# Kernel optimization log

Hardware: AMD Instinct MI355X
Metric: run time of the kernel (lower is better)

Reference implementation:

```python
import jax, jax.numpy as jnp
import numpy as np

IN_FEATURES = 4096
OUT_FEATURES = 4096
NNZ = 1677721  # int(4096*4096*(1-0.9))


def setup_inputs() -> dict:
    key = jax.random.key(0)
    k1, k2, k3, k4 = jax.random.split(key, 4)
    x = jax.random.normal(k1, (4, 2048, IN_FEATURES), dtype=jnp.float32)
    bound = 1.0 / np.sqrt(IN_FEATURES)
    sparse_values = jax.random.uniform(k2, (NNZ,), minval=-bound, maxval=bound, dtype=jnp.float32)
    bias = jax.random.uniform(k3, (OUT_FEATURES,), minval=-bound, maxval=bound, dtype=jnp.float32)
    flat_idx = jnp.sort(jax.random.randint(k4, (NNZ,), 0, IN_FEATURES * OUT_FEATURES, dtype=jnp.int64))
    return {"x": x, "sparse_values": sparse_values, "bias": bias, "flat_idx": flat_idx}


def reference(x, sparse_values, bias, flat_idx):
    # Fixed COO pattern: row = flat // in_features, col = flat % in_features
    rows = flat_idx // IN_FEATURES
    cols = flat_idx % IN_FEATURES
    # Scatter-add == COO coalesce (duplicates summed). W: [out, in]
    W = jnp.zeros((OUT_FEATURES, IN_FEATURES), dtype=sparse_values.dtype).at[rows, cols].add(sparse_values)
    # y = x W^T + b  (matches torch.sparse.mm(W, x^T)^T + b)
    y = jnp.einsum('bsi,oi->bso', x, W) + bias
    return y.astype(x.dtype)
```

## Files before the change

### kernel.cpp

```cpp
#include <hip/hip_runtime.h>
#include <hip/hip_bf16.h>
#include <stdint.h>

#define IN_F 4096
#define OUT_F 4096

typedef __attribute__((ext_vector_type(8))) __bf16 bf16x8;
typedef __attribute__((ext_vector_type(4))) float f32x4;

__device__ __forceinline__ void gl_lds_16(const void* g, void* l) {
    __builtin_amdgcn_global_load_lds((const __attribute__((address_space(1))) void*)g,
                                     (__attribute__((address_space(3))) void*)l,
                                     16, 0, 0);
}

__global__ void cvt_and_scatter(const float* __restrict__ x, __bf16* __restrict__ Xb, int n8,
                                const float* __restrict__ vals, const int* __restrict__ idx,
                                __bf16* __restrict__ W, int nnz, int cvtBlocks) {
    if ((int)blockIdx.x < cvtBlocks) {
        int i = blockIdx.x * blockDim.x + threadIdx.x;
        if (i < n8) {
            const float4* src = (const float4*)(x + (size_t)i * 8);
            float4 v0 = src[0], v1 = src[1];
            bf16x8 o;
            o[0] = (__bf16)v0.x; o[1] = (__bf16)v0.y; o[2] = (__bf16)v0.z; o[3] = (__bf16)v0.w;
            o[4] = (__bf16)v1.x; o[5] = (__bf16)v1.y; o[6] = (__bf16)v1.z; o[7] = (__bf16)v1.w;
            *(bf16x8*)(Xb + (size_t)i * 8) = o;
        }
    } else {
        int i = (blockIdx.x - cvtBlocks) * blockDim.x + threadIdx.x;
        if (i >= nnz) return;
        const int id = idx[i];
        if (i > 0 && idx[i - 1] == id) return;
        float s = vals[i];
        for (int j = i + 1; j < nnz && idx[j] == id; ++j) s += vals[j];
        W[id] = (__bf16)s;
    }
}

#define BM 256
#define BN 256
#define BK 32
#define NT (IN_F / BK)

__global__ __launch_bounds__(512, 2) void gemm_bf16_bt(
    const __bf16* __restrict__ A, const __bf16* __restrict__ B,
    const float* __restrict__ bias, float* __restrict__ C,
    int M, int N, int K)
{
    __shared__ __align__(128) __bf16 lds[4][16384];

    const int t512 = threadIdx.x;
    const int wave = t512 >> 6;
    const int lane = t512 & 63;
    const int wm = wave >> 2;
    const int wn = wave & 3;
    const int lq = lane >> 4;
    const int lr = lane & 15;

    const int bid  = blockIdx.x;
    const int wgid = (bid & 7) * 64 + (bid >> 3);
    const int mt = wgid >> 4;
    const int nt = wgid & 15;
    const int tileM = mt * BM;
    const int tileN = nt * BN;

    const int srow = t512 >> 2;
    const int scol = ((t512 & 3) ^ ((t512 >> 3) & 3)) * 8;

    const __bf16* gA0 = A + (size_t)(tileM + srow) * K + scol;
    const __bf16* gA1 = A + (size_t)(tileM + 128 + srow) * K + scol;
    const __bf16* gB0 = B + (size_t)(tileN + srow) * K + scol;
    const __bf16* gB1 = B + (size_t)(tileN + 128 + srow) * K + scol;

#define STAGE_A(buf, k0) do { \
        gl_lds_16(gA0 + (k0), &lds[buf][0]    + t512 * 8); \
        gl_lds_16(gA1 + (k0), &lds[buf][4096] + t512 * 8); } while (0)
#define STAGE_B(buf, k0) do { \
        gl_lds_16(gB0 + (k0), &lds[buf][8192]         + t512 * 8); \
        gl_lds_16(gB1 + (k0), &lds[buf][8192 + 4096]  + t512 * 8); } while (0)

    const int cswz = (lq ^ ((lr >> 1) & 3)) * 8;
    const int aoff = (wm * 128 + lr) * BK + cswz;
    const int boff = 8192 + (wn * 64 + lr) * BK + cswz;

    f32x4 acc[8][4] = {};
    bf16x8 fa0[8], fb0[4], fa1[8], fb1[4];

#define TILE_MAIN(T, FAc, FBc, FAn, FBn) do {                                   \
        const int t_ = (T);                                                     \
        const int pb_ = (t_ + 3) & 3; const int pk_ = (t_ + 3) * BK;            \
        STAGE_A(pb_, pk_); STAGE_B(pb_, pk_);                                   \
        const __bf16* nb_ = &lds[(t_ + 1) & 3][0];                              \
        _Pragma("unroll") for (int mi = 0; mi < 8; ++mi)                        \
            FAn[mi] = *(const bf16x8*)&nb_[aoff + mi * 512];                    \
        _Pragma("unroll") for (int ni = 0; ni < 4; ++ni)                        \
            FBn[ni] = *(const bf16x8*)&nb_[boff + ni * 512];                    \
        __builtin_amdgcn_s_setprio(1);                                          \
        _Pragma("unroll") for (int mi = 0; mi < 8; ++mi)                        \
            _Pragma("unroll") for (int ni = 0; ni < 4; ++ni)                    \
                acc[mi][ni] = __builtin_amdgcn_mfma_f32_16x16x32_bf16(          \
                    FAc[mi], FBc[ni], acc[mi][ni], 0, 0, 0);                    \
        __builtin_amdgcn_s_setprio(0);                                          \
        _Pragma("unroll") for (int g_ = 0; g_ < 4; ++g_) {                      \
            __builtin_amdgcn_sched_group_barrier(0x010, 1, 0);    \
            __builtin_amdgcn_sched_group_barrier(0x100, 3, 0);    \
            __builtin_amdgcn_sched_group_barrier(0x008, 8, 0);     \
        }                                                                       \
        asm volatile("s_waitcnt vmcnt(4)" ::: "memory");                        \
        __builtin_amdgcn_s_barrier();                                           \
        asm volatile("" ::: "memory");                                          \
    } while (0)

#define TILE(T, FAc, FBc, FAn, FBn) do {                                        \
        const int t_ = (T);                                                     \
        if (t_ + 3 < NT) {                                                      \
            const int pb_ = (t_ + 3) & 3; const int pk_ = (t_ + 3) * BK;        \
            STAGE_A(pb_, pk_); STAGE_B(pb_, pk_);                               \
        }                                                                       \
        if (t_ + 1 < NT) {                                                      \
            const __bf16* nb_ = &lds[(t_ + 1) & 3][0];                          \
            _Pragma("unroll") for (int mi = 0; mi < 8; ++mi)                    \
                FAn[mi] = *(const bf16x8*)&nb_[aoff + mi * 512];                \
            _Pragma("unroll") for (int ni = 0; ni < 4; ++ni)                    \
                FBn[ni] = *(const bf16x8*)&nb_[boff + ni * 512];                \
        }                                                                       \
        __builtin_amdgcn_s_setprio(1);                                          \
        _Pragma("unroll") for (int mi = 0; mi < 8; ++mi)                        \
            _Pragma("unroll") for (int ni = 0; ni < 4; ++ni)                    \
                acc[mi][ni] = __builtin_amdgcn_mfma_f32_16x16x32_bf16(          \
                    FAc[mi], FBc[ni], acc[mi][ni], 0, 0, 0);                    \
        __builtin_amdgcn_s_setprio(0);                                          \
        if (t_ < NT - 3)       asm volatile("s_waitcnt vmcnt(4)" ::: "memory"); \
        else if (t_ == NT - 3) asm volatile("s_waitcnt vmcnt(0)" ::: "memory"); \
        if (t_ < NT - 1) {                                                      \
            __builtin_amdgcn_s_barrier();                                       \
            asm volatile("" ::: "memory");                                      \
        }                                                                       \
    } while (0)

    STAGE_A(0, 0);   STAGE_B(0, 0);
    STAGE_A(1, 32);  STAGE_B(1, 32);
    STAGE_A(2, 64);  STAGE_B(2, 64);
    asm volatile("s_waitcnt vmcnt(4)" ::: "memory");
    __builtin_amdgcn_s_barrier();
    asm volatile("" ::: "memory");
    {
        const __bf16* nb_ = &lds[0][0];
#pragma unroll
        for (int mi = 0; mi < 8; ++mi) fa0[mi] = *(const bf16x8*)&nb_[aoff + mi * 512];
#pragma unroll
        for (int ni = 0; ni < 4; ++ni) fb0[ni] = *(const bf16x8*)&nb_[boff + ni * 512];
    }

    for (int t = 0; t < 124; t += 2) {
        TILE_MAIN(t,     fa0, fb0, fa1, fb1);
        TILE_MAIN(t + 1, fa1, fb1, fa0, fb0);
    }
    TILE(124, fa0, fb0, fa1, fb1);
    TILE(125, fa1, fb1, fa0, fb0);
    TILE(126, fa0, fb0, fa1, fb1);
    TILE(127, fa1, fb1, fa0, fb0);

    float bv[4];
#pragma unroll
    for (int ni = 0; ni < 4; ++ni) bv[ni] = bias[tileN + wn * 64 + ni * 16 + lr];
#pragma unroll
    for (int mi = 0; mi < 8; ++mi) {
#pragma unroll
        for (int ni = 0; ni < 4; ++ni) {
            const int gn = tileN + wn * 64 + ni * 16 + lr;
#pragma unroll
            for (int r = 0; r < 4; ++r) {
                const int gm = tileM + wm * 128 + mi * 16 + lq * 4 + r;
                C[(size_t)gm * N + gn] = acc[mi][ni][r] + bv[ni];
            }
        }
    }
#undef TILE
#undef TILE_MAIN
#undef STAGE_A
#undef STAGE_B
}

extern "C" void kernel_launch(void* const* d_in, const int* in_sizes, int n_in,
                              void* d_out, int out_size, void* d_ws, size_t ws_size,
                              hipStream_t stream) {
    const float* x    = (const float*)d_in[0];
    const float* vals = (const float*)d_in[1];
    const float* bias = (const float*)d_in[2];
    const int*   idx  = (const int*)d_in[3];
    float* out = (float*)d_out;

    const int nnz = in_sizes[1];
    const int K = IN_F, N = OUT_F;
    const int M = in_sizes[0] / K;

    char* ws = (char*)d_ws;
    __bf16* Wb = (__bf16*)ws;
    __bf16* Xb = (__bf16*)(ws + (size_t)32 * 1024 * 1024);

    const int wElems = N * K;
    const int xElems = M * K;
    const int n8 = xElems / 8;
    const int cvtBlocks = n8 / 256;
    const int scatBlocks = (nnz + 255) / 256;

    hipMemsetAsync(Wb, 0, (size_t)wElems * sizeof(__bf16), stream);
    cvt_and_scatter<<<cvtBlocks + scatBlocks, 256, 0, stream>>>(
        x, Xb, n8, vals, idx, Wb, nnz, cvtBlocks);

    gemm_bf16_bt<<<(M / BM) * (N / BN), 512, 0, stream>>>(Xb, Wb, bias, out, M, N, K);
}
```

Baseline: 463.6 us.

## Interleave global stages and LDS fragment loads with MFMA groups; split preprocessing kernels

The main GEMM tile loop now spreads the global-to-LDS staging for A and B and the per-fragment LDS reads across four chunks of MFMAs, each chunk being two row-blocks of four MFMAs. Before, all loads were issued up front and then the full MFMA block ran. Explicit sched_group_barrier sequences pin this interleaving, and the s_setprio calls around the MFMA block are removed. The fused convert/scatter kernel is also split into two separate launches. The goal is to hide LDS and VMEM issue latency behind matrix math, at the cost of one extra kernel launch and a schedule that depends on the compiler honouring the barriers.

```diff
diff --git a/kernel.cpp b/kernel.cpp
--- a/kernel.cpp
+++ b/kernel.cpp
@@ -14,28 +14,27 @@
                                      16, 0, 0);
 }
 
-__global__ void cvt_and_scatter(const float* __restrict__ x, __bf16* __restrict__ Xb, int n8,
-                                const float* __restrict__ vals, const int* __restrict__ idx,
-                                __bf16* __restrict__ W, int nnz, int cvtBlocks) {
-    if ((int)blockIdx.x < cvtBlocks) {
-        int i = blockIdx.x * blockDim.x + threadIdx.x;
-        if (i < n8) {
-            const float4* src = (const float4*)(x + (size_t)i * 8);
-            float4 v0 = src[0], v1 = src[1];
-            bf16x8 o;
-            o[0] = (__bf16)v0.x; o[1] = (__bf16)v0.y; o[2] = (__bf16)v0.z; o[3] = (__bf16)v0.w;
-            o[4] = (__bf16)v1.x; o[5] = (__bf16)v1.y; o[6] = (__bf16)v1.z; o[7] = (__bf16)v1.w;
-            *(bf16x8*)(Xb + (size_t)i * 8) = o;
-        }
-    } else {
-        int i = (blockIdx.x - cvtBlocks) * blockDim.x + threadIdx.x;
-        if (i >= nnz) return;
-        const int id = idx[i];
-        if (i > 0 && idx[i - 1] == id) return;
-        float s = vals[i];
-        for (int j = i + 1; j < nnz && idx[j] == id; ++j) s += vals[j];
-        W[id] = (__bf16)s;
-    }
+__global__ void cvt_x(const float* __restrict__ x, __bf16* __restrict__ Xb, int n8) {
+    int i = blockIdx.x * blockDim.x + threadIdx.x;
+    if (i < n8) {
+        const float4* src = (const float4*)(x + (size_t)i * 8);
+        float4 v0 = src[0], v1 = src[1];
+        bf16x8 o;
+        o[0] = (__bf16)v0.x; o[1] = (__bf16)v0.y; o[2] = (__bf16)v0.z; o[3] = (__bf16)v0.w;
+        o[4] = (__bf16)v1.x; o[5] = (__bf16)v1.y; o[6] = (__bf16)v1.z; o[7] = (__bf16)v1.w;
+        *(bf16x8*)(Xb + (size_t)i * 8) = o;
+    }
+}
+
+__global__ void scatter_w(const float* __restrict__ vals, const int* __restrict__ idx,
+                          __bf16* __restrict__ W, int nnz) {
+    int i = blockIdx.x * blockDim.x + threadIdx.x;
+    if (i >= nnz) return;
+    const int id = idx[i];
+    if (i > 0 && idx[i - 1] == id) return;
+    float s = vals[i];
+    for (int j = i + 1; j < nnz && idx[j] == id; ++j) s += vals[j];
+    W[id] = (__bf16)s;
 }
 
 #define BM 256
@@ -87,26 +86,52 @@
     f32x4 acc[8][4] = {};
     bf16x8 fa0[8], fb0[4], fa1[8], fb1[4];
 
+#define MM2(FAc, FBc, MI0, MI1) do {                                            \
+        _Pragma("unroll") for (int ni_ = 0; ni_ < 4; ++ni_)                     \
+            acc[MI0][ni_] = __builtin_amdgcn_mfma_f32_16x16x32_bf16(            \
+                FAc[MI0], FBc[ni_], acc[MI0][ni_], 0, 0, 0);                    \
+        _Pragma("unroll") for (int ni_ = 0; ni_ < 4; ++ni_)                     \
+            acc[MI1][ni_] = __builtin_amdgcn_mfma_f32_16x16x32_bf16(            \
+                FAc[MI1], FBc[ni_], acc[MI1][ni_], 0, 0, 0);                    \
+    } while (0)
+
 #define TILE_MAIN(T, FAc, FBc, FAn, FBn) do {                                   \
         const int t_ = (T);                                                     \
         const int pb_ = (t_ + 3) & 3; const int pk_ = (t_ + 3) * BK;            \
-        STAGE_A(pb_, pk_); STAGE_B(pb_, pk_);                                   \
         const __bf16* nb_ = &lds[(t_ + 1) & 3][0];                              \
-        _Pragma("unroll") for (int mi = 0; mi < 8; ++mi)                        \
-            FAn[mi] = *(const bf16x8*)&nb_[aoff + mi * 512];                    \
-        _Pragma("unroll") for (int ni = 0; ni < 4; ++ni)                        \
-            FBn[ni] = *(const bf16x8*)&nb_[boff + ni * 512];                    \
-        __builtin_amdgcn_s_setprio(1);                                          \
-        _Pragma("unroll") for (int mi = 0; mi < 8; ++mi)                        \
-            _Pragma("unroll") for (int ni = 0; ni < 4; ++ni)                    \
-                acc[mi][ni] = __builtin_amdgcn_mfma_f32_16x16x32_bf16(          \
-                    FAc[mi], FBc[ni], acc[mi][ni], 0, 0, 0);                    \
-        __builtin_amdgcn_s_setprio(0);                                          \
-        _Pragma("unroll") for (int g_ = 0; g_ < 4; ++g_) {                      \
-            __builtin_amdgcn_sched_group_barrier(0x010, 1, 0);    \
-            __builtin_amdgcn_sched_group_barrier(0x100, 3, 0);    \
-            __builtin_amdgcn_sched_group_barrier(0x008, 8, 0);     \
-        }                                                                       \
+                                                  \
+        STAGE_A(pb_, pk_);                                                      \
+        FAn[0] = *(const bf16x8*)&nb_[aoff];                                    \
+        FAn[1] = *(const bf16x8*)&nb_[aoff + 512];                              \
+        FBn[0] = *(const bf16x8*)&nb_[boff];                                    \
+        MM2(FAc, FBc, 0, 1);                                                    \
+                                                  \
+        STAGE_B(pb_, pk_);                                                      \
+        FBn[1] = *(const bf16x8*)&nb_[boff + 512];                              \
+        FBn[2] = *(const bf16x8*)&nb_[boff + 1024];                             \
+        FBn[3] = *(const bf16x8*)&nb_[boff + 1536];                             \
+        MM2(FAc, FBc, 2, 3);                                                    \
+                                                          \
+        FAn[2] = *(const bf16x8*)&nb_[aoff + 1024];                             \
+        FAn[3] = *(const bf16x8*)&nb_[aoff + 1536];                             \
+        FAn[4] = *(const bf16x8*)&nb_[aoff + 2048];                             \
+        MM2(FAc, FBc, 4, 5);                                                    \
+                                                          \
+        FAn[5] = *(const bf16x8*)&nb_[aoff + 2560];                             \
+        FAn[6] = *(const bf16x8*)&nb_[aoff + 3072];                             \
+        FAn[7] = *(const bf16x8*)&nb_[aoff + 3584];                             \
+        MM2(FAc, FBc, 6, 7);                                                    \
+           \
+        __builtin_amdgcn_sched_group_barrier(0x030, 2, 0);         \
+        __builtin_amdgcn_sched_group_barrier(0x100, 3, 0);         \
+        __builtin_amdgcn_sched_group_barrier(0x008, 8, 0);         \
+        __builtin_amdgcn_sched_group_barrier(0x030, 2, 0);                      \
+        __builtin_amdgcn_sched_group_barrier(0x100, 3, 0);                      \
+        __builtin_amdgcn_sched_group_barrier(0x008, 8, 0);                      \
+        __builtin_amdgcn_sched_group_barrier(0x100, 3, 0);                      \
+        __builtin_amdgcn_sched_group_barrier(0x008, 8, 0);                      \
+        __builtin_amdgcn_sched_group_barrier(0x100, 3, 0);                      \
+        __builtin_amdgcn_sched_group_barrier(0x008, 8, 0);                      \
         asm volatile("s_waitcnt vmcnt(4)" ::: "memory");                        \
         __builtin_amdgcn_s_barrier();                                           \
         asm volatile("" ::: "memory");                                          \
@@ -125,12 +150,10 @@
             _Pragma("unroll") for (int ni = 0; ni < 4; ++ni)                    \
                 FBn[ni] = *(const bf16x8*)&nb_[boff + ni * 512];                \
         }                                                                       \
-        __builtin_amdgcn_s_setprio(1);                                          \
         _Pragma("unroll") for (int mi = 0; mi < 8; ++mi)                        \
             _Pragma("unroll") for (int ni = 0; ni < 4; ++ni)                    \
                 acc[mi][ni] = __builtin_amdgcn_mfma_f32_16x16x32_bf16(          \
                     FAc[mi], FBc[ni], acc[mi][ni], 0, 0, 0);                    \
-        __builtin_amdgcn_s_setprio(0);                                          \
         if (t_ < NT - 3)       asm volatile("s_waitcnt vmcnt(4)" ::: "memory"); \
         else if (t_ == NT - 3) asm volatile("s_waitcnt vmcnt(0)" ::: "memory"); \
         if (t_ < NT - 1) {                                                      \
@@ -179,6 +202,7 @@
     }
 #undef TILE
 #undef TILE_MAIN
+#undef MM2
 #undef STAGE_A
 #undef STAGE_B
 }
@@ -207,8 +231,8 @@
     const int scatBlocks = (nnz + 255) / 256;
 
     hipMemsetAsync(Wb, 0, (size_t)wElems * sizeof(__bf16), stream);
-    cvt_and_scatter<<<cvtBlocks + scatBlocks, 256, 0, stream>>>(
-        x, Xb, n8, vals, idx, Wb, nnz, cvtBlocks);
+    cvt_x<<<cvtBlocks, 256, 0, stream>>>(x, Xb, n8);
+    scatter_w<<<scatBlocks, 256, 0, stream>>>(vals, idx, Wb, nnz);
 
     gemm_bf16_bt<<<(M / BM) * (N / BN), 512, 0, stream>>>(Xb, Wb, bias, out, M, N, K);
 }
```

Measured after the change: 453.5 us. 2.2% less time.
